# Optimization experiments

Measured on AMD Instinct MI355X. Metric: run time of the kernel, lower is better.

## Reference

```python
import jax, jax.numpy as jnp
import numpy as np


def setup_inputs() -> dict:
    key = jax.random.key(0)
    ks = jax.random.split(key, 5)
    B, S, C, H = 32, 512, 320, 512
    scale = 1.0 / np.sqrt(H)
    return {
        "x": jax.random.normal(ks[0], (B, S, C), dtype=jnp.float32),
        "w_ih": jax.random.normal(ks[1], (4 * H, S), dtype=jnp.float32) * scale,
        "w_hh": jax.random.normal(ks[2], (4 * H, H), dtype=jnp.float32) * scale,
        "b_ih": jax.random.normal(ks[3], (4 * H,), dtype=jnp.float32) * scale,
        "b_hh": jax.random.normal(ks[4], (4 * H,), dtype=jnp.float32) * scale,
    }


def reference(x, w_ih, w_hh, b_ih, b_hh):
    # x: (B, S, C). Original permutes to (B, C, S) and runs a length-1 LSTM per
    # channel with zero initial state -> single LSTM cell step:
    #   gates = x_c @ W_ih^T + b_ih + b_hh   (W_hh @ h0 == 0)
    # PyTorch gate order: i, f, g, o.
    B, S, C = x.shape
    H = w_hh.shape[1]
    gates = jnp.einsum("bsc,gs->bcg", x, w_ih) + b_ih + b_hh  # (B, C, 4H)
    i_g, f_g, g_g, o_g = jnp.split(gates, 4, axis=-1)
    c = jax.nn.sigmoid(i_g) * jnp.tanh(g_g)           # c0 = 0
    h = jax.nn.sigmoid(o_g) * jnp.tanh(c)             # (B, C, H)
    # Faithful to torch: cat over channels along batch dim -> (C*B, H),
    # then reshape to (B, C, H) (scrambles batch/channel order).
    h = jnp.transpose(h, (1, 0, 2)).reshape(B, C, H)
    # dropout is identity in eval mode
    return jnp.transpose(h, (0, 2, 1))                # (B, H, C)
```

## Files before the change

kernel.cpp:

```cpp
#include <hip/hip_runtime.h>
#include <stdint.h>

#define B_  32
#define S_  512
#define C_  320
#define H_  512
#define NROW (B_*C_)

typedef __attribute__((ext_vector_type(8))) short short8;
typedef __attribute__((ext_vector_type(4))) float f32x4;

__device__ __forceinline__ unsigned short f2bf(float x){
  unsigned u = __builtin_bit_cast(unsigned, x);
  u = u + 0x7FFFu + ((u >> 16) & 1u);
  return (unsigned short)(u >> 16);
}
__device__ __forceinline__ float bf2f(unsigned short h){
  unsigned u = ((unsigned)h) << 16;
  return __builtin_bit_cast(float, u);
}
__device__ __forceinline__ float sigf(float x){ return 1.0f/(1.0f + __expf(-x)); }
__device__ __forceinline__ float tanh_fast(float x){ return 2.0f/(1.0f + __expf(-2.0f*x)) - 1.0f; }

__global__ __launch_bounds__(256) void k_prep(const float* __restrict__ w,
                                              const float* __restrict__ x,
                                              unsigned short* __restrict__ aws,
                                              unsigned short* __restrict__ xws){
  const int bidg = blockIdx.x;
  const int tid = threadIdx.x;
  if (bidg < 768){
    int flat = bidg*256 + tid;
    int plane = flat >> 16;
    int rem   = flat & 65535;
    int srow  = (plane == 0 ? 0 : (plane == 1 ? 1024 : 1536));
    float4 v = ((const float4*)w)[srow*128 + rem];
    uint2 p;
    p.x = (unsigned)f2bf(v.x) | ((unsigned)f2bf(v.y) << 16);
    p.y = (unsigned)f2bf(v.z) | ((unsigned)f2bf(v.w) << 16);
    ((uint2*)aws)[flat] = p;
    return;
  }
  __shared__ float lds[64][65];
  const int idx = bidg - 768;
  const int st = idx & 7;
  const int r5 = idx >> 3;
  const int ctt = r5 % 5, b = r5 / 5;
  const int s0 = st*64, c0 = ctt*64;
  const int row = tid >> 2, q = tid & 3;

  const float* src = x + ((size_t)(b*S_ + s0 + row))*C_ + c0 + q*16;
  #pragma unroll
  for (int j = 0; j < 4; j++){
    float4 v = ((const float4*)src)[j];
    lds[row][q*16 + j*4 + 0] = v.x;
    lds[row][q*16 + j*4 + 1] = v.y;
    lds[row][q*16 + j*4 + 2] = v.z;
    lds[row][q*16 + j*4 + 3] = v.w;
  }
  __syncthreads();
  const int crow = row;
  #pragma unroll
  for (int j = 0; j < 2; j++){
    short8 o;
    #pragma unroll
    for (int e = 0; e < 8; e++)
      o[e] = (short)f2bf(lds[q*16 + j*8 + e][crow]);
    *(short8*)(xws + ((size_t)(b*C_ + c0 + crow))*S_ + s0 + q*16 + j*8) = o;
  }
}

__global__ __launch_bounds__(256, 2) void k_gemm(const unsigned short* __restrict__ aws,
                                                 const unsigned short* __restrict__ xws,
                                                 const float* __restrict__ b_ih,
                                                 const float* __restrict__ b_hh,
                                                 unsigned short* __restrict__ hws){
  __shared__ alignas(16) char lds[2][40960];

  const int tid  = threadIdx.x;
  const int w    = tid >> 6;
  const int lane = tid & 63;
  const int wm = w >> 1, wn = w & 1;

  const int bid = blockIdx.x;
  const int x8 = bid & 7, y = bid >> 3;
  const int kt = y & 7, n2 = y >> 3;
  const int nt = n2*8 + x8;
  const int k0 = kt*64;
  const int nbase = nt*128;

  f32x4 acc[3][2][4];
  #pragma unroll
  for (int gi = 0; gi < 3; gi++)
    #pragma unroll
    for (int mf = 0; mf < 2; mf++)
      #pragma unroll
      for (int nf = 0; nf < 4; nf++)
        acc[gi][mf][nf] = (f32x4){0.f, 0.f, 0.f, 0.f};

  const int cr   = lane >> 3;
  const int slot = ((lane & 7) ^ cr) << 4;

  const char* wsb = (const char*)aws;
  unsigned srcoff[10];
  int      dstoff[10];
  #pragma unroll
  for (int i = 0; i < 10; i++){
    int q = w*10 + i;
    if (q < 24){
      int gi = q >> 3, q8 = q & 7;
      int grow = gi*512 + k0 + q8*8 + cr;
      srcoff[i] = (unsigned)(grow*1024 + slot);
      dstoff[i] = gi*8192 + q8*1024 + (lane << 4);
    } else {
      int q8 = q - 24;
      int xrow = nbase + q8*8 + cr;
      srcoff[i] = (unsigned)(2097152 + xrow*1024 + slot);
      dstoff[i] = 24576 + q8*1024 + (lane << 4);
    }
  }

  short8 ld[10];
  #pragma unroll
  for (int i = 0; i < 10; i++)
    ld[i] = *(const short8*)(wsb + (size_t)srcoff[i]);
  #pragma unroll
  for (int i = 0; i < 10; i++)
    *(short8*)(&lds[0][0] + dstoff[i]) = ld[i];
  __syncthreads();

  const int lo16 = (lane >> 4) << 4;
  const int swz  = (lane & 7) << 4;
  const int l15  = lane & 15;

  #pragma unroll
  for (int t = 0; t < 8; t++){
    const int p = t & 1;
    char* base  = &lds[0][0] + p*40960;
    char* other = &lds[0][0] + (p^1)*40960;

    if (t < 7){
      #pragma unroll
      for (int i = 0; i < 10; i++)
        ld[i] = *(const short8*)(wsb + (size_t)(srcoff[i] + (unsigned)(t+1)*128));
      __builtin_amdgcn_sched_barrier(0);
    }

    #pragma unroll
    for (int ks = 0; ks < 2; ks++){
      const int colb = (ks*64 + lo16) ^ swz;
      short8 aF[3][2], bF[4];
      #pragma unroll
      for (int gi = 0; gi < 3; gi++)
        #pragma unroll
        for (int mf = 0; mf < 2; mf++)
          aF[gi][mf] = *(const short8*)(base + gi*8192 + (wm*32 + mf*16 + l15)*128 + colb);
      #pragma unroll
      for (int nf = 0; nf < 4; nf++)
        bF[nf] = *(const short8*)(base + 24576 + (wn*64 + nf*16 + l15)*128 + colb);
      #pragma unroll
      for (int gi = 0; gi < 3; gi++)
        #pragma unroll
        for (int mf = 0; mf < 2; mf++)
          #pragma unroll
          for (int nf = 0; nf < 4; nf++)
            acc[gi][mf][nf] = __builtin_amdgcn_mfma_f32_16x16x32_bf16(aF[gi][mf], bF[nf], acc[gi][mf][nf], 0, 0, 0);
    }

    if (t < 7){
      #pragma unroll
      for (int i = 0; i < 10; i++)
        *(short8*)(other + dstoff[i]) = ld[i];
    }
    __syncthreads();
  }

  #pragma unroll
  for (int mf = 0; mf < 2; mf++){
    const int kb = k0 + wm*32 + mf*16 + ((lane >> 4) << 2);
    float bi[4], bg[4], bo[4];
    #pragma unroll
    for (int r = 0; r < 4; r++){
      bi[r] = b_ih[kb + r]        + b_hh[kb + r];
      bg[r] = b_ih[1024 + kb + r] + b_hh[1024 + kb + r];
      bo[r] = b_ih[1536 + kb + r] + b_hh[1536 + kb + r];
    }
    #pragma unroll
    for (int nf = 0; nf < 4; nf++){
      const int n = nbase + wn*64 + nf*16 + l15;
      const int bb = n / 320;
      const int cc = n - bb*320;
      const size_t nr = (size_t)cc*32 + (size_t)bb;
      float h[4];
      #pragma unroll
      for (int r = 0; r < 4; r++){
        float iv = acc[0][mf][nf][r] + bi[r];
        float gv = acc[1][mf][nf][r] + bg[r];
        float ov = acc[2][mf][nf][r] + bo[r];
        float ce = sigf(iv) * tanh_fast(gv);
        h[r] = sigf(ov) * tanh_fast(ce);
      }
      uint2 p2;
      p2.x = (unsigned)f2bf(h[0]) | ((unsigned)f2bf(h[1]) << 16);
      p2.y = (unsigned)f2bf(h[2]) | ((unsigned)f2bf(h[3]) << 16);
      *(uint2*)(hws + nr*H_ + kb) = p2;
    }
  }
}

__global__ __launch_bounds__(256) void k_out(const unsigned short* __restrict__ hws,
                                             float* __restrict__ out){
  __shared__ float lds[64][65];
  const int tid = threadIdx.x;
  const int kt = blockIdx.x, ctt = blockIdx.y, b2 = blockIdx.z;
  const int k0 = kt*64, n0 = b2*320 + ctt*64;
  const int rr = tid >> 2, q = tid & 3;

  #pragma unroll
  for (int j = 0; j < 2; j++){
    short8 v = *(const short8*)(hws + ((size_t)(n0 + rr))*H_ + k0 + q*16 + j*8);
    #pragma unroll
    for (int e = 0; e < 8; e++)
      lds[rr][q*16 + j*8 + e] = bf2f((unsigned short)v[e]);
  }
  __syncthreads();
  const int krow = rr;
  #pragma unroll
  for (int j = 0; j < 4; j++){
    int c2l = q*16 + j*4;
    float4 o;
    o.x = lds[c2l + 0][krow];
    o.y = lds[c2l + 1][krow];
    o.z = lds[c2l + 2][krow];
    o.w = lds[c2l + 3][krow];
    *(float4*)(out + (size_t)b2*(H_*C_) + (size_t)(k0 + krow)*C_ + ctt*64 + c2l) = o;
  }
}

extern "C" void kernel_launch(void* const* d_in, const int* in_sizes, int n_in,
                              void* d_out, int out_size, void* d_ws, size_t ws_size,
                              hipStream_t stream){
  const float* x    = (const float*)d_in[0];
  const float* w_ih = (const float*)d_in[1];
  const float* b_ih = (const float*)d_in[3];
  const float* b_hh = (const float*)d_in[4];
  float* out = (float*)d_out;

  char* ws = (char*)d_ws;
  unsigned short* aws = (unsigned short*)(ws);
  unsigned short* xws = (unsigned short*)(ws + 2097152);
  unsigned short* hws = (unsigned short*)(ws + 2097152 + 10485760);

  k_prep <<<2048, 256, 0, stream>>>(w_ih, x, aws, xws);
  k_gemm <<<640, 256, 0, stream>>>(aws, xws, b_ih, b_hh, hws);
  k_out  <<<dim3(8, 5, 32), 256, 0, stream>>>(hws, out);
}
```

Baseline: 53.57 us.

## Give each wave its own GEMM tile using direct global-to-LDS loads

The GEMM stops sharing a 128x128 block tile across four waves. Each wave now owns a 32x64 tile in a private LDS region, fed by global_load_lds (direct global-to-LDS) instructions, so the block-wide __syncthreads and the register round-trip for staging go away. The prep kernel writes x rows already in the scrambled channel-major order, which removes the divide/mod index math from the GEMM epilogue. In exchange, waves no longer share A/B tiles, so global and L2 traffic per FLOP goes up, and each wave uses a single LDS buffer with explicit waitcnt fences instead of double buffering.

New measurement: 56.69 us. +5.8%, slower.

```diff
diff --git a/kernel.cpp b/kernel.cpp
--- a/kernel.cpp
+++ b/kernel.cpp
@@ -5,15 +5,14 @@
 #define S_  512
 #define C_  320
 #define H_  512
-#define NROW (B_*C_)
 
 typedef __attribute__((ext_vector_type(8))) short short8;
 typedef __attribute__((ext_vector_type(4))) float f32x4;
 
-__device__ __forceinline__ unsigned short f2bf(float x){
+__device__ __forceinline__ unsigned f2bf(float x){
   unsigned u = __builtin_bit_cast(unsigned, x);
   u = u + 0x7FFFu + ((u >> 16) & 1u);
-  return (unsigned short)(u >> 16);
+  return u >> 16;
 }
 __device__ __forceinline__ float bf2f(unsigned short h){
   unsigned u = ((unsigned)h) << 16;
@@ -21,6 +20,11 @@
 }
 __device__ __forceinline__ float sigf(float x){ return 1.0f/(1.0f + __expf(-x)); }
 __device__ __forceinline__ float tanh_fast(float x){ return 2.0f/(1.0f + __expf(-2.0f*x)) - 1.0f; }
+
+__device__ __forceinline__ void gload16(const void* g, void* l){
+  __builtin_amdgcn_global_load_lds((const __attribute__((address_space(1))) void*)g,
+                                   (__attribute__((address_space(3))) void*)l, 16, 0, 0);
+}
 
 __global__ __launch_bounds__(256) void k_prep(const float* __restrict__ w,
                                               const float* __restrict__ x,
@@ -35,8 +39,8 @@
     int srow  = (plane == 0 ? 0 : (plane == 1 ? 1024 : 1536));
     float4 v = ((const float4*)w)[srow*128 + rem];
     uint2 p;
-    p.x = (unsigned)f2bf(v.x) | ((unsigned)f2bf(v.y) << 16);
-    p.y = (unsigned)f2bf(v.z) | ((unsigned)f2bf(v.w) << 16);
+    p.x = f2bf(v.x) | (f2bf(v.y) << 16);
+    p.y = f2bf(v.z) | (f2bf(v.w) << 16);
     ((uint2*)aws)[flat] = p;
     return;
   }
@@ -58,14 +62,17 @@
     lds[row][q*16 + j*4 + 3] = v.w;
   }
   __syncthreads();
-  const int crow = row;
-  #pragma unroll
-  for (int j = 0; j < 2; j++){
+  const int wr2 = tid >> 3;
+  const int l8  = tid & 7;
+  #pragma unroll
+  for (int half = 0; half < 2; half++){
+    const int crow = half*32 + wr2;
+    const size_t nprime = (size_t)(c0 + crow)*32 + (size_t)b;
     short8 o;
     #pragma unroll
     for (int e = 0; e < 8; e++)
-      o[e] = (short)f2bf(lds[q*16 + j*8 + e][crow]);
-    *(short8*)(xws + ((size_t)(b*C_ + c0 + crow))*S_ + s0 + q*16 + j*8) = o;
+      o[e] = (short)f2bf(lds[l8*8 + e][crow]);
+    *(short8*)(xws + nprime*S_ + s0 + l8*8) = o;
   }
 }
 
@@ -74,19 +81,18 @@
                                                  const float* __restrict__ b_ih,
                                                  const float* __restrict__ b_hh,
                                                  unsigned short* __restrict__ hws){
-  __shared__ alignas(16) char lds[2][40960];
+  __shared__ alignas(16) char lds[4][20480];
 
   const int tid  = threadIdx.x;
   const int w    = tid >> 6;
   const int lane = tid & 63;
-  const int wm = w >> 1, wn = w & 1;
-
-  const int bid = blockIdx.x;
-  const int x8 = bid & 7, y = bid >> 3;
-  const int kt = y & 7, n2 = y >> 3;
-  const int nt = n2*8 + x8;
-  const int k0 = kt*64;
-  const int nbase = nt*128;
+  char* wb = &lds[w][0];
+
+  const int wt = blockIdx.x*4 + w;
+  const int mt = wt & 15;
+  const int nt = wt >> 4;
+  const int k0 = mt*32;
+  const int nbase = nt*64;
 
   f32x4 acc[3][2][4];
   #pragma unroll
@@ -101,32 +107,26 @@
   const int slot = ((lane & 7) ^ cr) << 4;
 
   const char* wsb = (const char*)aws;
-  unsigned srcoff[10];
-  int      dstoff[10];
-  #pragma unroll
-  for (int i = 0; i < 10; i++){
-    int q = w*10 + i;
-    if (q < 24){
-      int gi = q >> 3, q8 = q & 7;
+  unsigned srcoff[20];
+  #pragma unroll
+  for (int i = 0; i < 20; i++){
+    if (i < 12){
+      int gi = i >> 2, q8 = i & 3;
       int grow = gi*512 + k0 + q8*8 + cr;
       srcoff[i] = (unsigned)(grow*1024 + slot);
-      dstoff[i] = gi*8192 + q8*1024 + (lane << 4);
     } else {
-      int q8 = q - 24;
+      int q8 = i - 12;
       int xrow = nbase + q8*8 + cr;
       srcoff[i] = (unsigned)(2097152 + xrow*1024 + slot);
-      dstoff[i] = 24576 + q8*1024 + (lane << 4);
-    }
-  }
-
-  short8 ld[10];
-  #pragma unroll
-  for (int i = 0; i < 10; i++)
-    ld[i] = *(const short8*)(wsb + (size_t)srcoff[i]);
-  #pragma unroll
-  for (int i = 0; i < 10; i++)
-    *(short8*)(&lds[0][0] + dstoff[i]) = ld[i];
-  __syncthreads();
+    }
+  }
+
+  #pragma unroll
+  for (int i = 0; i < 20; i++){
+    const int d = (i < 12) ? ((i >> 2)*4096 + (i & 3)*1024) : (12288 + (i - 12)*1024);
+    gload16(wsb + (size_t)srcoff[i], wb + d);
+    srcoff[i] += 128;
+  }
 
   const int lo16 = (lane >> 4) << 4;
   const int swz  = (lane & 7) << 4;
@@ -134,49 +134,49 @@
 
   #pragma unroll
   for (int t = 0; t < 8; t++){
-    const int p = t & 1;
-    char* base  = &lds[0][0] + p*40960;
-    char* other = &lds[0][0] + (p^1)*40960;
-
-    if (t < 7){
-      #pragma unroll
-      for (int i = 0; i < 10; i++)
-        ld[i] = *(const short8*)(wsb + (size_t)(srcoff[i] + (unsigned)(t+1)*128));
-      __builtin_amdgcn_sched_barrier(0);
-    }
-
+    asm volatile("s_waitcnt vmcnt(0)" ::: "memory");
+    __builtin_amdgcn_sched_barrier(0);
+
+    short8 aF[2][3][2], bF[2][4];
     #pragma unroll
     for (int ks = 0; ks < 2; ks++){
       const int colb = (ks*64 + lo16) ^ swz;
-      short8 aF[3][2], bF[4];
       #pragma unroll
       for (int gi = 0; gi < 3; gi++)
         #pragma unroll
         for (int mf = 0; mf < 2; mf++)
-          aF[gi][mf] = *(const short8*)(base + gi*8192 + (wm*32 + mf*16 + l15)*128 + colb);
+          aF[ks][gi][mf] = *(const short8*)(wb + gi*4096 + (mf*16 + l15)*128 + colb);
       #pragma unroll
       for (int nf = 0; nf < 4; nf++)
-        bF[nf] = *(const short8*)(base + 24576 + (wn*64 + nf*16 + l15)*128 + colb);
+        bF[ks][nf] = *(const short8*)(wb + 12288 + (nf*16 + l15)*128 + colb);
+    }
+    asm volatile("s_waitcnt lgkmcnt(0)" ::: "memory");
+    __builtin_amdgcn_sched_barrier(0);
+
+    if (t < 7){
+      #pragma unroll
+      for (int i = 0; i < 20; i++){
+        const int d = (i < 12) ? ((i >> 2)*4096 + (i & 3)*1024) : (12288 + (i - 12)*1024);
+        gload16(wsb + (size_t)srcoff[i], wb + d);
+        srcoff[i] += 128;
+      }
+      __builtin_amdgcn_sched_barrier(0);
+    }
+
+    #pragma unroll
+    for (int ks = 0; ks < 2; ks++)
       #pragma unroll
       for (int gi = 0; gi < 3; gi++)
         #pragma unroll
         for (int mf = 0; mf < 2; mf++)
           #pragma unroll
           for (int nf = 0; nf < 4; nf++)
-            acc[gi][mf][nf] = __builtin_amdgcn_mfma_f32_16x16x32_bf16(aF[gi][mf], bF[nf], acc[gi][mf][nf], 0, 0, 0);
-    }
-
-    if (t < 7){
-      #pragma unroll
-      for (int i = 0; i < 10; i++)
-        *(short8*)(other + dstoff[i]) = ld[i];
-    }
-    __syncthreads();
+            acc[gi][mf][nf] = __builtin_amdgcn_mfma_f32_16x16x32_bf16(aF[ks][gi][mf], bF[ks][nf], acc[gi][mf][nf], 0, 0, 0);
   }
 
   #pragma unroll
   for (int mf = 0; mf < 2; mf++){
-    const int kb = k0 + wm*32 + mf*16 + ((lane >> 4) << 2);
+    const int kb = k0 + mf*16 + ((lane >> 4) << 2);
     float bi[4], bg[4], bo[4];
     #pragma unroll
     for (int r = 0; r < 4; r++){
@@ -186,10 +186,7 @@
     }
     #pragma unroll
     for (int nf = 0; nf < 4; nf++){
-      const int n = nbase + wn*64 + nf*16 + l15;
-      const int bb = n / 320;
-      const int cc = n - bb*320;
-      const size_t nr = (size_t)cc*32 + (size_t)bb;
+      const int n = nbase + nf*16 + l15;
       float h[4];
       #pragma unroll
       for (int r = 0; r < 4; r++){
@@ -200,9 +197,9 @@
         h[r] = sigf(ov) * tanh_fast(ce);
       }
       uint2 p2;
-      p2.x = (unsigned)f2bf(h[0]) | ((unsigned)f2bf(h[1]) << 16);
-      p2.y = (unsigned)f2bf(h[2]) | ((unsigned)f2bf(h[3]) << 16);
-      *(uint2*)(hws + nr*H_ + kb) = p2;
+      p2.x = f2bf(h[0]) | (f2bf(h[1]) << 16);
+      p2.y = f2bf(h[2]) | (f2bf(h[3]) << 16);
+      *(uint2*)(hws + (size_t)n*H_ + kb) = p2;
     }
   }
 }
@@ -248,7 +245,7 @@
   char* ws = (char*)d_ws;
   unsigned short* aws = (unsigned short*)(ws);
   unsigned short* xws = (unsigned short*)(ws + 2097152);
-  unsigned short* hws = (unsigned short*)(ws + 2097152 + 10485760);
+  unsigned short* hws = (unsigned short*)(ws + 12582912);
 
   k_prep <<<2048, 256, 0, stream>>>(w_ih, x, aws, xws);
   k_gemm <<<640, 256, 0, stream>>>(aws, xws, b_ih, b_hh, hws);
```
